# Optimization experiments

Measured on AMD Instinct MI355X. Metric: run time of the kernel, lower is better.

The kernel has to match this reference:

```python
import jax, jax.numpy as jnp
import numpy as np

ATOM, BOND, INNER, HID, REC, OHID = 14, 3, 20, 34, 20, 25
N_NODES = 1048576
N_EDGES = 983040
MAX_DEPTH = 16
N_GRAPHS = 16384


def leaky(x):
    return jnp.where(x >= 0, x, 0.01 * x)


def setup_inputs() -> dict:
    key = jax.random.key(0)
    ks = jax.random.split(key, 20)
    p = 0.02
    atom_feats = jax.random.normal(ks[0], (N_NODES, ATOM), jnp.float32)
    bond_feats = jax.random.normal(ks[1], (N_EDGES, BOND), jnp.float32)
    # build a forest: node i's parent is some node with strictly smaller depth.
    # For a jit-friendly synthetic instance we assign depths and connect each
    # non-root node (edge) from a parent at depth d to child at depth d+1.
    depth = np.asarray(jax.random.randint(ks[2], (N_NODES,), 0, MAX_DEPTH))
    order = np.argsort(depth, kind='stable')
    depth_sorted = depth[order]
    # edges: child must have depth >= 1; pick children among nodes with depth>0
    child_pool = order[depth_sorted > 0]
    rng = np.random.default_rng(0)
    child_idx = rng.choice(child_pool, size=N_EDGES, replace=False) if len(child_pool) >= N_EDGES else rng.choice(child_pool, size=N_EDGES, replace=True)
    child_depth = depth[child_idx]
    # parent: random node with depth == child_depth - 1
    # bucket nodes by depth
    buckets = [order[depth_sorted == d] for d in range(MAX_DEPTH)]
    parent_idx = np.empty(N_EDGES, dtype=np.int64)
    for d in range(1, MAX_DEPTH):
        m = child_depth == d
        if m.sum() > 0:
            parent_idx[m] = rng.choice(buckets[d - 1], size=int(m.sum()))
    graph_id = np.asarray(jax.random.randint(ks[3], (N_NODES,), 0, N_GRAPHS))
    # roots: nodes with no incoming edge (not a child)
    is_child = np.zeros(N_NODES, dtype=bool)
    is_child[child_idx] = True
    is_root = (~is_child).astype(np.float32)
    params = {
        'inner_w': jax.random.normal(ks[4], (REC + BOND, INNER), jnp.float32) * p,
        'inner_b': jnp.zeros((INNER,), jnp.float32),
        'net_w1': jax.random.normal(ks[5], (INNER + ATOM, HID), jnp.float32) * p,
        'net_b1': jnp.zeros((HID,), jnp.float32),
        'net_w2': jax.random.normal(ks[6], (HID, REC), jnp.float32) * p,
        'net_b2': jnp.zeros((REC,), jnp.float32),
        'net0_w1': jax.random.normal(ks[7], (ATOM, HID), jnp.float32) * p,
        'net0_b1': jnp.zeros((HID,), jnp.float32),
        'net0_w2': jax.random.normal(ks[8], (HID, REC), jnp.float32) * p,
        'net0_b2': jnp.zeros((REC,), jnp.float32),
        'out_w1': jax.random.normal(ks[9], (REC, OHID), jnp.float32) * p,
        'out_b1': jnp.zeros((OHID,), jnp.float32),
        'out_w2': jax.random.normal(ks[10], (OHID, 1), jnp.float32) * p,
        'out_b2': jnp.zeros((1,), jnp.float32),
    }
    return dict(atom_feats=atom_feats, bond_feats=bond_feats,
                parent_idx=jnp.asarray(parent_idx), child_idx=jnp.asarray(child_idx),
                node_depth=jnp.asarray(depth), graph_id=jnp.asarray(graph_id),
                is_root=jnp.asarray(is_root), **params)


def reference(atom_feats, bond_feats, parent_idx, child_idx, node_depth, graph_id,
              is_root, inner_w, inner_b, net_w1, net_b1, net_w2, net_b2,
              net0_w1, net0_b1, net0_w2, net0_b2, out_w1, out_b1, out_w2, out_b2):
    n_nodes = atom_feats.shape[0]
    has_child = jnp.zeros((n_nodes,), jnp.float32).at[parent_idx].add(1.0) > 0
    # leaf vector via net0
    leaf_vec = leaky(leaky(atom_feats @ net0_w1 + net0_b1) @ net0_w2 + net0_b2)  # [N, REC]
    h = leaf_vec  # node recursive vectors; internal nodes filled bottom-up
    # process depths from deepest-1 parents up to 0: at step d, update nodes at depth d
    for d in range(MAX_DEPTH - 2, -1, -1):
        child_h = h[child_idx]  # [E, REC]
        msg = leaky(jnp.concatenate([bond_feats, child_h], axis=1) @ inner_w + inner_b)  # [E, INNER]
        # only edges whose parent is at depth d contribute this step
        edge_mask = (node_depth[parent_idx] == d).astype(msg.dtype)[:, None]
        inner_sum = jnp.zeros((n_nodes, INNER), msg.dtype).at[parent_idx].add(msg * edge_mask)
        x = jnp.concatenate([atom_feats, inner_sum], axis=1)  # [N, ATOM+INNER]
        new_h = leaky(leaky(x @ net_w1 + net_b1) @ net_w2 + net_b2)
        upd = ((node_depth == d) & has_child).astype(h.dtype)[:, None]
        h = h * (1.0 - upd) + new_h * upd
    # sum root vectors per graph
    root_h = h * is_root[:, None]
    g = jax.ops.segment_sum(root_h, graph_id, num_segments=N_GRAPHS)  # [G, REC]
    out = jnp.tanh(g @ out_w1 + out_b1) @ out_w2 + out_b2  # [G, 1]
    return out.reshape(-1)
```

## Files before the change

kernel.cpp:

```cpp
#include <hip/hip_runtime.h>

#define ATOM  14
#define BOND  3
#define INNER 20
#define HID   34
#define HIDP  36
#define REC   20
#define OHID  25
#define NN    1048576
#define NE    983040
#define NG    16384

#define NB    512
#define NT    256
#define GT    (NB*NT)
#define SPAN  (NN/NB)
#define SE    (SPAN/NT)

#define NB2   1024
#define NT2   256
#define NGRP  (NT2/4)
#define SSTR  (NGRP+1)
#define NBINS (NB2*32)

__device__ __forceinline__ float leaky(float x) { return x >= 0.f ? x : 0.01f * x; }

__device__ __forceinline__ void wsync() {
    __builtin_amdgcn_wave_barrier();
    __builtin_amdgcn_sched_barrier(0);
}

__device__ __forceinline__ void gbar_f(int* bar, int goal) {
    __syncthreads();
    if (threadIdx.x == 0) {
        __threadfence();
        __hip_atomic_fetch_add(bar, 1, __ATOMIC_RELEASE, __HIP_MEMORY_SCOPE_AGENT);
        while (__hip_atomic_load(bar, __ATOMIC_RELAXED, __HIP_MEMORY_SCOPE_AGENT) < goal)
            __builtin_amdgcn_s_sleep(32);
        __threadfence();
    }
    __syncthreads();
}

__global__ void k_pre(int* cnt_n, int2* pnode2, float* g, int* bin_cnt, int* totals, int* bars) {
    int tid = blockIdx.x * 256 + threadIdx.x;
    for (int i = tid; i < NN; i += 262144) { cnt_n[i] = 0; pnode2[i] = make_int2(i, -1); }
    for (int i = tid; i < NG * REC; i += 262144) g[i] = 0.f;
    for (int i = tid; i < NBINS; i += 262144) bin_cnt[i] = 0;
    if (tid == 0) { totals[0] = 0; totals[16] = 0; }
    if (tid == 1) for (int k = 0; k < 32; ++k) bars[k] = 0;
}

__global__ __launch_bounds__(NT) void k_prep(
    const int* __restrict__ parent, const int* __restrict__ child,
    const int* __restrict__ depth, const int* __restrict__ gid,
    const float* __restrict__ isr,
    int* cnt_n, int2* pnode2, int* inv, int* K_s,
    int4* nodeinfo, int* row_ptr, int* adjc,
    int* bin_cnt, int* bin_base, int* bin_cur,
    int* totals, int* bar)
{
    __shared__ int sh[NT];
    __shared__ int sbase_sh;
    const int t = threadIdx.x;
    const int tid = blockIdx.x * NT + t;
    int ep = 0;

    for (int e = tid; e < NE; e += GT) {
        atomicAdd(&cnt_n[parent[e]], 1);
        pnode2[child[e]] = make_int2(parent[e], e);
    }
    gbar_f(bar, NB * ++ep);

    for (int i = tid; i < NN; i += GT) {
        int d = depth[i];
        int r = i;
        for (int s = 0; s < d; ++s) r = pnode2[r].x;
        int K = (r & (NB2 - 1)) * 32 + d * 2 + (cnt_n[i] == 0 ? 1 : 0);
        K_s[i] = K;
        atomicAdd(&bin_cnt[K], 1);
    }
    gbar_f(bar, NB * ++ep);

    if (blockIdx.x < NBINS / NT) {
        int k0 = blockIdx.x * NT + t;
        int v = bin_cnt[k0];
        sh[t] = v;
        __syncthreads();
        for (int ofs = 1; ofs < NT; ofs <<= 1) {
            int x = (t >= ofs) ? sh[t - ofs] : 0;
            __syncthreads();
            sh[t] += x;
            __syncthreads();
        }
        if (t == NT - 1) sbase_sh = atomicAdd(&totals[0], sh[t]);
        __syncthreads();
        int b = sbase_sh + sh[t] - v;
        bin_base[k0] = b;
        bin_cur[k0] = b;
    }
    gbar_f(bar, NB * ++ep);

    for (int i = tid; i < NN; i += GT) {
        int pos = atomicAdd(&bin_cur[K_s[i]], 1);
        int2 pe = pnode2[i];
        int gr = (isr[i] != 0.f) ? gid[i] : -1;
        nodeinfo[pos] = make_int4(i, cnt_n[i], gr, pe.y);
        inv[i] = pos;
    }
    gbar_f(bar, NB * ++ep);

    {
        int base0 = blockIdx.x * SPAN + t * SE;
        int v[SE]; int sum = 0;
        #pragma unroll
        for (int k = 0; k < SE; ++k) { v[k] = nodeinfo[base0 + k].y; sum += v[k]; }
        __syncthreads();
        sh[t] = sum;
        __syncthreads();
        for (int ofs = 1; ofs < NT; ofs <<= 1) {
            int x = (t >= ofs) ? sh[t - ofs] : 0;
            __syncthreads();
            sh[t] += x;
            __syncthreads();
        }
        if (t == NT - 1) sbase_sh = atomicAdd(&totals[16], sh[t]);
        __syncthreads();
        int run = sbase_sh + sh[t] - sum;
        #pragma unroll
        for (int k = 0; k < SE; ++k) { row_ptr[base0 + k] = run; cnt_n[base0 + k] = run; run += v[k]; }
    }
    gbar_f(bar, NB * ++ep);

    for (int pos = tid; pos < NN; pos += GT) {
        int4 ni = nodeinfo[pos];
        if (ni.w >= 0) {
            int ppn = pnode2[ni.x].x;
            int pp  = inv[ppn];
            int slot = atomicAdd(&cnt_n[pp], 1);
            adjc[slot] = pos;
        }
    }
}

__device__ __forceinline__ void coop_mlp(int slot, int j, int KN,
                                         const float* xs, float* hs, float* os,
                                         const float* w1, const float* b1,
                                         const float* w2, const float* b2,
                                         float* o)
{
    wsync();
    float acc[9];
    #pragma unroll
    for (int u = 0; u < 9; ++u) { int h = 9*j + u; acc[u] = (h < HID) ? b1[h] : 0.f; }
    #pragma unroll 2
    for (int k = 0; k < KN; ++k) {
        float xk = xs[k * SSTR + slot];
        #pragma unroll
        for (int u = 0; u < 9; ++u) { int h = 9*j + u; if (h < HID) acc[u] += xk * w1[k * HIDP + h]; }
    }
    #pragma unroll
    for (int u = 0; u < 9; ++u) { int h = 9*j + u; if (h < HID) hs[h * SSTR + slot] = leaky(acc[u]); }
    wsync();
    #pragma unroll
    for (int u = 0; u < 5; ++u) o[u] = b2[5*j + u];
    #pragma unroll 2
    for (int k = 0; k < HID; ++k) {
        float hk = hs[k * SSTR + slot];
        #pragma unroll
        for (int u = 0; u < 5; ++u) o[u] += hk * w2[k * REC + 5*j + u];
    }
    #pragma unroll
    for (int u = 0; u < 5; ++u) { o[u] = leaky(o[u]); os[(5*j + u) * SSTR + slot] = o[u]; }
    wsync();
}

__global__ __launch_bounds__(NT2) void k_levels(
    const float* __restrict__ atom, const float* __restrict__ bond,
    const int4* __restrict__ nodeinfo, const int* __restrict__ row_ptr,
    const int* __restrict__ adjc,
    const int* __restrict__ bin_base, const int* __restrict__ bin_cnt,
    const float* __restrict__ iw, const float* __restrict__ ib,
    const float* __restrict__ nw1, const float* __restrict__ nb1,
    const float* __restrict__ nw2, const float* __restrict__ nb2,
    const float* __restrict__ l0w1, const float* __restrict__ l0b1,
    const float* __restrict__ l0w2, const float* __restrict__ l0b2,
    float* __restrict__ g, float* __restrict__ msg_s)
{
    __shared__ float lw1[34 * HIDP];
    __shared__ float lw2[HID * REC];
    __shared__ float liw[23 * REC];
    __shared__ float zw1[ATOM * HIDP];
    __shared__ float zw2[HID * REC];
    __shared__ float lb1[HID], lb2[REC], lbi[INNER], zb1[HID], zb2[REC];
    __shared__ float xs[34 * SSTR];
    __shared__ float hs[34 * SSTR];
    __shared__ float os[20 * SSTR];

    const int t = threadIdx.x;
    const int b = blockIdx.x;
    const int slot = t >> 2;
    const int j = t & 3;

    for (int idx = t; idx < 34 * HIDP; idx += NT2) {
        int r = idx / HIDP, c = idx - r * HIDP;
        lw1[idx] = (c < HID) ? nw1[r * HID + c] : 0.f;
    }
    for (int idx = t; idx < HID * REC; idx += NT2) { lw2[idx] = nw2[idx]; zw2[idx] = l0w2[idx]; }
    for (int idx = t; idx < 23 * REC; idx += NT2) liw[idx] = iw[idx];
    for (int idx = t; idx < ATOM * HIDP; idx += NT2) {
        int r = idx / HIDP, c = idx - r * HIDP;
        zw1[idx] = (c < HID) ? l0w1[r * HID + c] : 0.f;
    }
    if (t < HID) { lb1[t] = nb1[t]; zb1[t] = l0b1[t]; }
    else if (t >= 64 && t < 64 + REC) { lb2[t - 64] = nb2[t - 64]; zb2[t - 64] = l0b2[t - 64]; }
    if (t >= 96 && t < 96 + INNER) lbi[t - 96] = ib[t - 96];
    __syncthreads();

    for (int d = 15; d >= 0; --d) {
        {
            int K = b * 32 + d * 2;
            int base = bin_base[K], n0 = bin_cnt[K];
            for (int idx = slot; idx < n0; idx += NGRP) {
                int pos = base + idx;
                int4 ni = nodeinfo[pos];
                int rp0 = row_ptr[pos];
                float s0 = 0.f, s1 = 0.f, s2 = 0.f, s3 = 0.f, s4 = 0.f;
                for (int r = rp0; r < rp0 + ni.y; ++r) {
                    const float* mp = msg_s + (size_t)adjc[r] * REC + 5*j;
                    s0 += mp[0]; s1 += mp[1]; s2 += mp[2]; s3 += mp[3]; s4 += mp[4];
                }
                const float* ar = atom + (size_t)ni.x * ATOM;
                #pragma unroll
                for (int u = 0; u < 4; ++u) { int k = 4*j + u; if (k < ATOM) xs[k * SSTR + slot] = ar[k]; }
                xs[(ATOM + 5*j + 0) * SSTR + slot] = s0;
                xs[(ATOM + 5*j + 1) * SSTR + slot] = s1;
                xs[(ATOM + 5*j + 2) * SSTR + slot] = s2;
                xs[(ATOM + 5*j + 3) * SSTR + slot] = s3;
                xs[(ATOM + 5*j + 4) * SSTR + slot] = s4;
                float o[5];
                coop_mlp(slot, j, ATOM + INNER, xs, hs, os, lw1, lb1, lw2, lb2, o);
                if (ni.z >= 0) {
                    #pragma unroll
                    for (int u = 0; u < 5; ++u) atomicAdd(&g[(size_t)ni.z * REC + 5*j + u], o[u]);
                } else {
                    const float* br = bond + (size_t)ni.w * BOND;
                    float b0 = br[0], b1 = br[1], b2 = br[2];
                    float m[5];
                    #pragma unroll
                    for (int u = 0; u < 5; ++u)
                        m[u] = lbi[5*j + u] + b0 * liw[0 * INNER + 5*j + u]
                             + b1 * liw[1 * INNER + 5*j + u] + b2 * liw[2 * INNER + 5*j + u];
                    #pragma unroll 2
                    for (int k = 0; k < REC; ++k) {
                        float ok = os[k * SSTR + slot];
                        #pragma unroll
                        for (int u = 0; u < 5; ++u) m[u] += ok * liw[(BOND + k) * INNER + 5*j + u];
                    }
                    #pragma unroll
                    for (int u = 0; u < 5; ++u) msg_s[(size_t)pos * REC + 5*j + u] = leaky(m[u]);
                }
            }
        }
        {
            int K = b * 32 + d * 2 + 1;
            int base = bin_base[K], n1 = bin_cnt[K];
            for (int idx = slot; idx < n1; idx += NGRP) {
                int pos = base + idx;
                int4 ni = nodeinfo[pos];
                const float* ar = atom + (size_t)ni.x * ATOM;
                #pragma unroll
                for (int u = 0; u < 4; ++u) { int k = 4*j + u; if (k < ATOM) xs[k * SSTR + slot] = ar[k]; }
                float o[5];
                coop_mlp(slot, j, ATOM, xs, hs, os, zw1, zb1, zw2, zb2, o);
                if (ni.z >= 0) {
                    #pragma unroll
                    for (int u = 0; u < 5; ++u) atomicAdd(&g[(size_t)ni.z * REC + 5*j + u], o[u]);
                } else {
                    const float* br = bond + (size_t)ni.w * BOND;
                    float b0 = br[0], b1 = br[1], b2 = br[2];
                    float m[5];
                    #pragma unroll
                    for (int u = 0; u < 5; ++u)
                        m[u] = lbi[5*j + u] + b0 * liw[0 * INNER + 5*j + u]
                             + b1 * liw[1 * INNER + 5*j + u] + b2 * liw[2 * INNER + 5*j + u];
                    #pragma unroll 2
                    for (int k = 0; k < REC; ++k) {
                        float ok = os[k * SSTR + slot];
                        #pragma unroll
                        for (int u = 0; u < 5; ++u) m[u] += ok * liw[(BOND + k) * INNER + 5*j + u];
                    }
                    #pragma unroll
                    for (int u = 0; u < 5; ++u) msg_s[(size_t)pos * REC + 5*j + u] = leaky(m[u]);
                }
            }
        }
        __threadfence_block();
        __syncthreads();
    }
}

__global__ void k_out(const float* __restrict__ g,
                      const float* __restrict__ w1, const float* __restrict__ b1,
                      const float* __restrict__ w2, const float* __restrict__ b2,
                      float* __restrict__ out) {
    int t = blockIdx.x * 256 + threadIdx.x;
    if (t >= NG) return;
    const float* gv = g + (size_t)t * REC;
    float gl[REC];
    #pragma unroll
    for (int k = 0; k < REC; ++k) gl[k] = gv[k];
    float acc = b2[0];
    for (int j = 0; j < OHID; ++j) {
        float s = b1[j];
        #pragma unroll
        for (int k = 0; k < REC; ++k) s += gl[k] * w1[k * OHID + j];
        acc += tanhf(s) * w2[j];
    }
    out[t] = acc;
}

extern "C" void kernel_launch(void* const* d_in, const int* in_sizes, int n_in,
                              void* d_out, int out_size, void* d_ws, size_t ws_size,
                              hipStream_t stream) {
    const float* atom    = (const float*)d_in[0];
    const float* bond    = (const float*)d_in[1];
    const int*   parent  = (const int*)d_in[2];
    const int*   child   = (const int*)d_in[3];
    const int*   depth   = (const int*)d_in[4];
    const int*   gid     = (const int*)d_in[5];
    const float* isr     = (const float*)d_in[6];
    const float* inner_w = (const float*)d_in[7];
    const float* inner_b = (const float*)d_in[8];
    const float* net_w1  = (const float*)d_in[9];
    const float* net_b1  = (const float*)d_in[10];
    const float* net_w2  = (const float*)d_in[11];
    const float* net_b2  = (const float*)d_in[12];
    const float* net0_w1 = (const float*)d_in[13];
    const float* net0_b1 = (const float*)d_in[14];
    const float* net0_w2 = (const float*)d_in[15];
    const float* net0_b2 = (const float*)d_in[16];
    const float* out_w1  = (const float*)d_in[17];
    const float* out_b1  = (const float*)d_in[18];
    const float* out_w2  = (const float*)d_in[19];
    const float* out_b2  = (const float*)d_in[20];
    float* out = (float*)d_out;

    char* ws = (char*)d_ws;
    size_t o = 0;
    float* msg_s    = (float*)(ws + o);  o += (size_t)NN * REC * 4;
    int4* nodeinfo  = (int4*)(ws + o);   o += (size_t)NN * 16;
    float* g        = (float*)(ws + o);  o += (size_t)NG * REC * 4;
    int2* pnode2    = (int2*)(ws + o);   o += (size_t)NN * 8;
    int* adjc       = (int*)(ws + o);    o += (size_t)NE * 4;
    int* cnt_n      = (int*)(ws + o);    o += (size_t)NN * 4;
    int* inv        = (int*)(ws + o);    o += (size_t)NN * 4;
    int* K_s        = (int*)(ws + o);    o += (size_t)NN * 4;
    int* row_ptr    = (int*)(ws + o);    o += (size_t)NN * 4;
    int* bin_cnt    = (int*)(ws + o);    o += (size_t)NBINS * 4;
    int* bin_base   = (int*)(ws + o);    o += (size_t)NBINS * 4;
    int* bin_cur    = (int*)(ws + o);    o += (size_t)NBINS * 4;
    int* totals     = (int*)(ws + o);    o += 32 * 4;
    int* bars       = (int*)(ws + o);    o += 32 * 4;

    k_pre<<<1024, 256, 0, stream>>>(cnt_n, pnode2, g, bin_cnt, totals, bars);
    k_prep<<<NB, NT, 0, stream>>>(parent, child, depth, gid, isr,
                                  cnt_n, pnode2, inv, K_s, nodeinfo, row_ptr,
                                  adjc, bin_cnt, bin_base, bin_cur, totals, bars);
    k_levels<<<NB2, NT2, 0, stream>>>(atom, bond, nodeinfo, row_ptr, adjc,
                                      bin_base, bin_cnt,
                                      inner_w, inner_b, net_w1, net_b1, net_w2, net_b2,
                                      net0_w1, net0_b1, net0_w2, net0_b2,
                                      g, msg_s);
    k_out<<<(NG + 255) / 256, 256, 0, stream>>>(g, out_w1, out_b1, out_w2, out_b2, out);
}
```

Measured before the change: 951.7 us.

## Build CSR in original node order and pack row/count into nodeinfo

Builds the child-adjacency CSR row offsets from a scan over original node indices instead of over sorted positions. Each child's slot within its parent comes from the atomic rank captured when counting edges, which removes the inv array and the second atomic fill pass. It also merges the scatter pass into the scan pass, saving one grid barrier. Row start and child count are packed into nodeinfo.w, so k_levels no longer reads row_ptr. The bit packing assumes fewer than 4096 children per node, an edge index below 2^20, and row offsets below 2^20. The adjacency order is now nondeterministic from the atomic ranks, and the sum order varies with it.

```diff
diff --git a/kernel.cpp b/kernel.cpp
--- a/kernel.cpp
+++ b/kernel.cpp
@@ -14,8 +14,7 @@
 #define NB    512
 #define NT    256
 #define GT    (NB*NT)
-#define SPAN  (NN/NB)
-#define SE    (SPAN/NT)
+#define NIT   (NN/GT)
 
 #define NB2   1024
 #define NT2   256
@@ -55,8 +54,8 @@
     const int* __restrict__ parent, const int* __restrict__ child,
     const int* __restrict__ depth, const int* __restrict__ gid,
     const float* __restrict__ isr,
-    int* cnt_n, int2* pnode2, int* inv, int* K_s,
-    int4* nodeinfo, int* row_ptr, int* adjc,
+    int* cnt_n, int2* pnode2, int* K_s,
+    int4* nodeinfo, int* row_n, int* adjc,
     int* bin_cnt, int* bin_base, int* bin_cur,
     int* totals, int* bar)
 {
@@ -67,8 +66,9 @@
     int ep = 0;
 
     for (int e = tid; e < NE; e += GT) {
-        atomicAdd(&cnt_n[parent[e]], 1);
-        pnode2[child[e]] = make_int2(parent[e], e);
+        int p = parent[e];
+        int r = atomicAdd(&cnt_n[p], 1);
+        pnode2[child[e]] = make_int2(p, (r << 20) | e);
     }
     gbar_f(bar, NB * ++ep);
 
@@ -101,22 +101,11 @@
     }
     gbar_f(bar, NB * ++ep);
 
-    for (int i = tid; i < NN; i += GT) {
-        int pos = atomicAdd(&bin_cur[K_s[i]], 1);
-        int2 pe = pnode2[i];
-        int gr = (isr[i] != 0.f) ? gid[i] : -1;
-        nodeinfo[pos] = make_int4(i, cnt_n[i], gr, pe.y);
-        inv[i] = pos;
-    }
-    gbar_f(bar, NB * ++ep);
-
-    {
-        int base0 = blockIdx.x * SPAN + t * SE;
-        int v[SE]; int sum = 0;
-        #pragma unroll
-        for (int k = 0; k < SE; ++k) { v[k] = nodeinfo[base0 + k].y; sum += v[k]; }
-        __syncthreads();
-        sh[t] = sum;
+    for (int k = 0; k < NIT; ++k) {
+        int i = tid + k * GT;
+        int cn = cnt_n[i];
+        __syncthreads();
+        sh[t] = cn;
         __syncthreads();
         for (int ofs = 1; ofs < NT; ofs <<= 1) {
             int x = (t >= ofs) ? sh[t - ofs] : 0;
@@ -126,18 +115,21 @@
         }
         if (t == NT - 1) sbase_sh = atomicAdd(&totals[16], sh[t]);
         __syncthreads();
-        int run = sbase_sh + sh[t] - sum;
-        #pragma unroll
-        for (int k = 0; k < SE; ++k) { row_ptr[base0 + k] = run; cnt_n[base0 + k] = run; run += v[k]; }
+        int row = sbase_sh + sh[t] - cn;
+        int pos = atomicAdd(&bin_cur[K_s[i]], 1);
+        int2 pe = pnode2[i];
+        int gr = (isr[i] != 0.f) ? gid[i] : -1;
+        nodeinfo[pos] = make_int4(i, pe.y, gr, (row << 12) | cn);
+        row_n[i] = row;
     }
     gbar_f(bar, NB * ++ep);
 
     for (int pos = tid; pos < NN; pos += GT) {
         int4 ni = nodeinfo[pos];
-        if (ni.w >= 0) {
+        if (ni.z < 0) {
             int ppn = pnode2[ni.x].x;
-            int pp  = inv[ppn];
-            int slot = atomicAdd(&cnt_n[pp], 1);
+            int rank = ((unsigned)ni.y) >> 20;
+            int slot = row_n[ppn] + rank;
             adjc[slot] = pos;
         }
     }
@@ -177,8 +169,7 @@
 
 __global__ __launch_bounds__(NT2) void k_levels(
     const float* __restrict__ atom, const float* __restrict__ bond,
-    const int4* __restrict__ nodeinfo, const int* __restrict__ row_ptr,
-    const int* __restrict__ adjc,
+    const int4* __restrict__ nodeinfo, const int* __restrict__ adjc,
     const int* __restrict__ bin_base, const int* __restrict__ bin_cnt,
     const float* __restrict__ iw, const float* __restrict__ ib,
     const float* __restrict__ nw1, const float* __restrict__ nb1,
@@ -224,9 +215,10 @@
             for (int idx = slot; idx < n0; idx += NGRP) {
                 int pos = base + idx;
                 int4 ni = nodeinfo[pos];
-                int rp0 = row_ptr[pos];
+                int n   = ni.w & 0xFFF;
+                int rp0 = ((unsigned)ni.w) >> 12;
                 float s0 = 0.f, s1 = 0.f, s2 = 0.f, s3 = 0.f, s4 = 0.f;
-                for (int r = rp0; r < rp0 + ni.y; ++r) {
+                for (int r = rp0; r < rp0 + n; ++r) {
                     const float* mp = msg_s + (size_t)adjc[r] * REC + 5*j;
                     s0 += mp[0]; s1 += mp[1]; s2 += mp[2]; s3 += mp[3]; s4 += mp[4];
                 }
@@ -244,7 +236,7 @@
                     #pragma unroll
                     for (int u = 0; u < 5; ++u) atomicAdd(&g[(size_t)ni.z * REC + 5*j + u], o[u]);
                 } else {
-                    const float* br = bond + (size_t)ni.w * BOND;
+                    const float* br = bond + (size_t)(ni.y & 0xFFFFF) * BOND;
                     float b0 = br[0], b1 = br[1], b2 = br[2];
                     float m[5];
                     #pragma unroll
@@ -277,7 +269,7 @@
                     #pragma unroll
                     for (int u = 0; u < 5; ++u) atomicAdd(&g[(size_t)ni.z * REC + 5*j + u], o[u]);
                 } else {
-                    const float* br = bond + (size_t)ni.w * BOND;
+                    const float* br = bond + (size_t)(ni.y & 0xFFFFF) * BOND;
                     float b0 = br[0], b1 = br[1], b2 = br[2];
                     float m[5];
                     #pragma unroll
@@ -354,9 +346,8 @@
     int2* pnode2    = (int2*)(ws + o);   o += (size_t)NN * 8;
     int* adjc       = (int*)(ws + o);    o += (size_t)NE * 4;
     int* cnt_n      = (int*)(ws + o);    o += (size_t)NN * 4;
-    int* inv        = (int*)(ws + o);    o += (size_t)NN * 4;
+    int* row_n      = (int*)(ws + o);    o += (size_t)NN * 4;
     int* K_s        = (int*)(ws + o);    o += (size_t)NN * 4;
-    int* row_ptr    = (int*)(ws + o);    o += (size_t)NN * 4;
     int* bin_cnt    = (int*)(ws + o);    o += (size_t)NBINS * 4;
     int* bin_base   = (int*)(ws + o);    o += (size_t)NBINS * 4;
     int* bin_cur    = (int*)(ws + o);    o += (size_t)NBINS * 4;
@@ -365,9 +356,9 @@
 
     k_pre<<<1024, 256, 0, stream>>>(cnt_n, pnode2, g, bin_cnt, totals, bars);
     k_prep<<<NB, NT, 0, stream>>>(parent, child, depth, gid, isr,
-                                  cnt_n, pnode2, inv, K_s, nodeinfo, row_ptr,
+                                  cnt_n, pnode2, K_s, nodeinfo, row_n,
                                   adjc, bin_cnt, bin_base, bin_cur, totals, bars);
-    k_levels<<<NB2, NT2, 0, stream>>>(atom, bond, nodeinfo, row_ptr, adjc,
+    k_levels<<<NB2, NT2, 0, stream>>>(atom, bond, nodeinfo, adjc,
                                       bin_base, bin_cnt,
                                       inner_w, inner_b, net_w1, net_b1, net_w2, net_b2,
                                       net0_w1, net0_b1, net0_w2, net0_b2,
```

New measurement: 894.8 us, median of 2. -6.0%, faster.
